# Performance work log

Measured on AMD Instinct MI355X. Metric: run time of the kernel, lower is better.

Reference implementation:

```python
import jax, jax.numpy as jnp
import numpy as np

C = 256
HEADS = 8
HEAD_DIM = C // HEADS
SCALE = HEAD_DIM ** -0.5
POOL = 2
LN_EPS = 1e-5


def setup_inputs() -> dict:
    key = jax.random.key(0)
    ks = jax.random.split(key, 10)
    B, H, W = 8, 64, 64
    std = 0.02
    return {
        "x": jax.random.normal(ks[0], (B, C, H, W), jnp.float32),
        "Wq": jax.random.normal(ks[1], (HEADS, C), jnp.float32) * std,
        "Wk": jax.random.normal(ks[2], (HEADS, C), jnp.float32) * std,
        "Wv": jax.random.normal(ks[3], (C, C), jnp.float32) * std,
        "Wsr": jax.random.normal(ks[4], (C, C), jnp.float32) * (2.0 / C) ** 0.5,
        "bsr": jnp.zeros((C,), jnp.float32),
        "gamma": jnp.ones((C,), jnp.float32),
        "beta": jnp.zeros((C,), jnp.float32),
        "Wp": jax.random.normal(ks[5], (C, C), jnp.float32) * std,
        "bp": jnp.zeros((C,), jnp.float32),
    }


def reference(x, Wq, Wk, Wv, Wsr, bsr, gamma, beta, Wp, bp):
    B, Cc, H, W = x.shape
    N = H * W
    # tokens [B, N, C]
    tok = x.reshape(B, Cc, N).transpose(0, 2, 1)
    # q: Linear(C -> heads), per-head scalar query  [B, heads, N]
    q = jnp.einsum("bnc,hc->bhn", tok, Wq)
    # spatial reduction: avgpool(pool_ratio) then 1x1 conv
    xp = x.reshape(B, Cc, H // POOL, POOL, W // POOL, POOL).mean(axis=(3, 5))
    xs = jnp.einsum("bchw,oc->bohw", xp, Wsr) + bsr[None, :, None, None]
    M = (H // POOL) * (W // POOL)
    x_ = xs.reshape(B, Cc, M).transpose(0, 2, 1)  # [B, M, C]
    # LayerNorm + GELU (exact erf, torch default)
    mu = x_.mean(-1, keepdims=True)
    var = ((x_ - mu) ** 2).mean(-1, keepdims=True)
    x_ = (x_ - mu) * jax.lax.rsqrt(var + LN_EPS) * gamma + beta
    x_ = jax.nn.gelu(x_, approximate=False)
    # k: per-head scalar key [B, heads, M]; v: [B, heads, M, head_dim]
    k = jnp.einsum("bmc,hc->bhm", x_, Wk)
    v = jnp.einsum("bmc,oc->bmo", x_, Wv).reshape(B, M, HEADS, HEAD_DIM).transpose(0, 2, 1, 3)
    # rank-1 attention scores [B, heads, N, M]
    attn = jax.nn.softmax(q[:, :, :, None] * k[:, :, None, :] * SCALE, axis=-1)
    out = jnp.einsum("bhnm,bhmd->bhnd", attn, v)  # [B, heads, N, head_dim]
    out = out.transpose(0, 2, 1, 3).reshape(B, N, Cc)
    out = out @ Wp.T + bp
    return out.transpose(0, 2, 1).reshape(B, Cc, H, W)
```

## Files before the change

### kernel.cpp

```cpp
#include <hip/hip_runtime.h>
#include <math.h>


#define NH 8
#define NJ 8
#define NT (NH * NJ)
#define SCALE 0.17677669529663687f

__device__ __constant__ float INVFACT[NJ] = {
    1.0f, 1.0f, 0.5f, 1.6666666666666666e-01f, 4.1666666666666664e-02f,
    8.3333333333333332e-03f, 1.3888888888888889e-03f, 1.9841269841269841e-04f};

__global__ void k0_q_prep(const float* __restrict__ x, const float* __restrict__ Wq,
                          const float* __restrict__ Wsr, const float* __restrict__ Wv,
                          float* __restrict__ q01, float* __restrict__ WsrT,
                          float* __restrict__ WvT) {
    __shared__ float wq[NH * 128];
    const int tid = threadIdx.x;
    const int blk = blockIdx.x;
    if (blk < 256) {
        const int b = blk >> 5, half = (blk >> 4) & 1, nt = blk & 15;
#pragma unroll
        for (int r = 0; r < 4; ++r) {
            int idx = r * 256 + tid;
            int h = idx >> 7, cc = idx & 127;
            wq[idx] = Wq[h * 256 + half * 128 + cc];
        }
        __syncthreads();
        const int n = nt * 256 + tid;
        const float* xb = x + (((size_t)b << 8) + half * 128) * 4096 + n;
        float acc[NH] = {};
#pragma unroll 8
        for (int c = 0; c < 128; ++c) {
            float xv = xb[(size_t)c << 12];
#pragma unroll
            for (int h = 0; h < NH; ++h) acc[h] += xv * wq[h * 128 + c];
        }
#pragma unroll
        for (int h = 0; h < NH; ++h)
            q01[((size_t)(half * 64 + b * 8 + h) << 12) + n] = acc[h];
    } else {
        const float* W = (blk < 288) ? Wsr : Wv;
        float* WT = (blk < 288) ? WsrT : WvT;
        const int c0 = (blk & 31) * 8;
#pragma unroll
        for (int r = 0; r < 2; ++r) {
            int fidx = r * 256 + tid;
            int c = c0 + (fidx >> 6), o4 = (fidx & 63) * 4;
            float4 t;
            t.x = W[(size_t)(o4 + 0) * 256 + c];
            t.y = W[(size_t)(o4 + 1) * 256 + c];
            t.z = W[(size_t)(o4 + 2) * 256 + c];
            t.w = W[(size_t)(o4 + 3) * 256 + c];
            *(float4*)&WT[(size_t)c * 256 + o4] = t;
        }
    }
}

__global__ __launch_bounds__(512, 1) void ka_mega(
        const float* __restrict__ x, const float* __restrict__ WsrT,
        const float* __restrict__ bsr, const float* __restrict__ WvT,
        const float* __restrict__ gamma, const float* __restrict__ beta,
        const float* __restrict__ Wk,
        float* __restrict__ Mpart, float* __restrict__ Spart) {
    __shared__ float smem[28800];
    float* a_pool = smem;
    float* wpan   = smem + 1152;
    float* g_lds  = smem + 9472;
    float* g_t    = smem + 17792;
    float4* wkv   = (float4*)(smem + 25984);
    float4* glv   = (float4*)(smem + 28032);
    float4* blv   = (float4*)(smem + 28288);
    float* klds   = smem + 28544;

    const int tid = threadIdx.x;
    const int blk = blockIdx.x;
    const int b = blk >> 5, mt = blk & 31;
    const int i2 = mt;

    const int ccs = tid >> 3, jg = tid & 7;
    const int mg = tid & 7, og = tid >> 3;

    wkv[tid] = ((const float4*)Wk)[tid];
    if (tid < 64) {
        glv[tid] = ((const float4*)gamma)[tid];
        blv[tid] = ((const float4*)beta)[tid];
    }

    float acc[4][4] = {};
    for (int c0 = 0; c0 < 256; c0 += 32) {
        __syncthreads();
        if (tid < 256) {
            const float* p = x + ((size_t)(b * 256 + c0 + ccs) << 12) +
                             i2 * 128 + jg * 8;
            float4 r00 = *(const float4*)p;
            float4 r01 = *(const float4*)(p + 4);
            float4 r10 = *(const float4*)(p + 64);
            float4 r11 = *(const float4*)(p + 68);
            float4 pv;
            pv.x = 0.25f * ((r00.x + r00.y) + (r10.x + r10.y));
            pv.y = 0.25f * ((r00.z + r00.w) + (r10.z + r10.w));
            pv.z = 0.25f * ((r01.x + r01.y) + (r11.x + r11.y));
            pv.w = 0.25f * ((r01.z + r01.w) + (r11.z + r11.w));
            *(float4*)&a_pool[ccs * 36 + jg * 4] = pv;
        }
#pragma unroll
        for (int r = 0; r < 4; ++r) {
            int fidx = r * 512 + tid;
            int cc = fidx >> 6, o4 = (fidx & 63) * 4;
            *(float4*)&wpan[cc * 260 + o4] =
                *(const float4*)&WsrT[(size_t)(c0 + cc) * 256 + o4];
        }
        __syncthreads();
#pragma unroll
        for (int cc = 0; cc < 32; ++cc) {
            float4 av = *(const float4*)&a_pool[cc * 36 + mg * 4];
            float4 bv = *(const float4*)&wpan[cc * 260 + og * 4];
            float am[4] = {av.x, av.y, av.z, av.w};
            float bo[4] = {bv.x, bv.y, bv.z, bv.w};
#pragma unroll
            for (int i = 0; i < 4; ++i)
#pragma unroll
                for (int j = 0; j < 4; ++j) acc[i][j] += am[i] * bo[j];
        }
    }
    {
        float4 bs = *(const float4*)&bsr[og * 4];
#pragma unroll
        for (int i = 0; i < 4; ++i) {
            float4 w0;
            w0.x = acc[i][0] + bs.x; w0.y = acc[i][1] + bs.y;
            w0.z = acc[i][2] + bs.z; w0.w = acc[i][3] + bs.w;
            *(float4*)&g_lds[(mg * 4 + i) * 260 + og * 4] = w0;
        }
    }
    __syncthreads();

    const int wave = tid >> 6, lane = tid & 63;
    {
        const float4 g4 = glv[lane], be4 = blv[lane];
        float4 wkreg[NH];
#pragma unroll
        for (int h = 0; h < NH; ++h) wkreg[h] = wkv[h * 64 + lane];
        const int w2 = wave >> 1, h2 = wave & 1;
        const int s = lane & 7;
        const int cb = ((w2 ^ (s >> 1)) << 3) | ((s & 1) << 2);
        const int cbh = cb ^ (h2 << 2);
        const int r0 = (lane * 4) << 5;
        float4 gg4[4];
#pragma unroll
        for (int ti = 0; ti < 4; ++ti) {
            const int mm = wave * 4 + ti;
            float4 vv = *(const float4*)&g_lds[mm * 260 + lane * 4];
            float ssum = (vv.x + vv.y) + (vv.z + vv.w);
            float s2 = (vv.x * vv.x + vv.y * vv.y) + (vv.z * vv.z + vv.w * vv.w);
#pragma unroll
            for (int off = 1; off < 64; off <<= 1) {
                ssum += __shfl_xor(ssum, off);
                s2 += __shfl_xor(s2, off);
            }
            const float mu = ssum * (1.f / 256.f);
            const float rstd = rsqrtf(s2 * (1.f / 256.f) - mu * mu + 1e-5f);
            float4 gg;
            {
                float xh;
                xh = (vv.x - mu) * rstd * g4.x + be4.x;
                gg.x = 0.5f * xh * (1.f + erff(xh * 0.70710678118654752f));
                xh = (vv.y - mu) * rstd * g4.y + be4.y;
                gg.y = 0.5f * xh * (1.f + erff(xh * 0.70710678118654752f));
                xh = (vv.z - mu) * rstd * g4.z + be4.z;
                gg.z = 0.5f * xh * (1.f + erff(xh * 0.70710678118654752f));
                xh = (vv.w - mu) * rstd * g4.w + be4.w;
                gg.w = 0.5f * xh * (1.f + erff(xh * 0.70710678118654752f));
            }
            gg4[ti] = gg;
            float acck[NH];
#pragma unroll
            for (int h = 0; h < NH; ++h) {
                float4 w = wkreg[h];
                acck[h] = (gg.x * w.x + gg.y * w.y) + (gg.z * w.z + gg.w * w.w);
            }
#pragma unroll
            for (int off = 1; off < 64; off <<= 1)
#pragma unroll
                for (int h = 0; h < NH; ++h) acck[h] += __shfl_xor(acck[h], off);
            if (lane == 0) {
#pragma unroll
                for (int h = 0; h < NH; ++h) klds[h * 32 + mm] = acck[h];
            }
        }
        float4 t;
#define GT_WRITE(K, COMP)                                                   \
        t.x = gg4[0].COMP; t.y = gg4[1].COMP;                               \
        t.z = gg4[2].COMP; t.w = gg4[3].COMP;                               \
        *(float4*)&g_t[r0 + ((K) << 5) + cbh] = t;
        GT_WRITE(0, x) GT_WRITE(1, y) GT_WRITE(2, z) GT_WRITE(3, w)
#undef GT_WRITE
    }

    float accv[4][4] = {};
    for (int c0 = 0; c0 < 256; c0 += 32) {
        __syncthreads();
#pragma unroll
        for (int r = 0; r < 4; ++r) {
            int fidx = r * 512 + tid;
            int cc = fidx >> 6, o4 = (fidx & 63) * 4;
            *(float4*)&wpan[cc * 260 + o4] =
                *(const float4*)&WvT[(size_t)(c0 + cc) * 256 + o4];
        }
        __syncthreads();
#pragma unroll
        for (int cc = 0; cc < 32; ++cc) {
            const int c = c0 + cc;
            const int swzc = ((c >> 2) & 7) << 2;
            float4 av = *(const float4*)&g_t[(c << 5) + ((mg << 2) ^ swzc)];
            float4 bv = *(const float4*)&wpan[cc * 260 + og * 4];
            float am[4] = {av.x, av.y, av.z, av.w};
            float bo[4] = {bv.x, bv.y, bv.z, bv.w};
#pragma unroll
            for (int i = 0; i < 4; ++i)
#pragma unroll
                for (int j = 0; j < 4; ++j) accv[i][j] += am[i] * bo[j];
        }
    }

    {
        const int h = og >> 3;
        float km[4], pw[4];
#pragma unroll
        for (int i = 0; i < 4; ++i) {
            km[i] = klds[h * 32 + mg * 4 + i];
            pw[i] = 1.f;
        }
        float sacc[NJ];
        float* Mrow = Mpart + ((size_t)blk << 11) + og * 4;
#pragma unroll
        for (int j = 0; j < NJ; ++j) {
            float mo[4];
#pragma unroll
            for (int o = 0; o < 4; ++o)
                mo[o] = (pw[0] * accv[0][o] + pw[1] * accv[1][o]) +
                        (pw[2] * accv[2][o] + pw[3] * accv[3][o]);
            float sj = (pw[0] + pw[1]) + (pw[2] + pw[3]);
#pragma unroll
            for (int i = 0; i < 4; ++i) pw[i] *= km[i];
#pragma unroll
            for (int off = 1; off < 8; off <<= 1) {
#pragma unroll
                for (int o = 0; o < 4; ++o) mo[o] += __shfl_xor(mo[o], off);
                sj += __shfl_xor(sj, off);
            }
            sacc[j] = sj;
            if (mg == 0) {
                float4 w0;
                w0.x = mo[0]; w0.y = mo[1]; w0.z = mo[2]; w0.w = mo[3];
                *(float4*)&Mrow[j * 256] = w0;
            }
        }
        if (mg == 0 && (og & 7) == 0) {
            float* Srow = Spart + ((size_t)blk << 6) + h * 8;
            float4 s0, s1;
            s0.x = sacc[0]; s0.y = sacc[1]; s0.z = sacc[2]; s0.w = sacc[3];
            s1.x = sacc[4]; s1.y = sacc[5]; s1.z = sacc[6]; s1.w = sacc[7];
            *(float4*)&Srow[0] = s0;
            *(float4*)&Srow[4] = s1;
        }
    }
}

__global__ void kc_fold(const float* __restrict__ Mpart,
                        const float* __restrict__ Spart,
                        const float* __restrict__ Wp,
                        float* __restrict__ P, float* __restrict__ S2) {
    const int bh = blockIdx.x;
    const int h = bh & 7, b = bh >> 3;
    const int tid = threadIdx.x;
    __shared__ float Ms[NJ][33];
    {
        const int j = tid >> 5, d = tid & 31;
        const float* src = Mpart + (((size_t)(b * 32) * 8 + j) << 8) + h * 32 + d;
        float s = 0.f;
#pragma unroll 8
        for (int mtn = 0; mtn < 32; ++mtn) s += src[(size_t)mtn << 11];
        Ms[j][d] = s * INVFACT[j];
    }
    if (tid < NJ) {
        const float* src = Spart + ((size_t)(b * 32) << 6) + h * 8 + tid;
        float ss = 0.f;
#pragma unroll 8
        for (int mtn = 0; mtn < 32; ++mtn) ss += src[mtn << 6];
        S2[bh * NJ + tid] = ss * INVFACT[tid];
    }
    __syncthreads();
    const int c = tid;
    float wp[32];
    const float* wrow = Wp + c * 256 + h * 32;
#pragma unroll
    for (int i = 0; i < 8; ++i) {
        float4 t = *(const float4*)(wrow + i * 4);
        wp[i * 4 + 0] = t.x; wp[i * 4 + 1] = t.y;
        wp[i * 4 + 2] = t.z; wp[i * 4 + 3] = t.w;
    }
#pragma unroll
    for (int j = 0; j < NJ; ++j) {
        float s = 0.f;
#pragma unroll
        for (int dd = 0; dd < 32; ++dd) s += wp[dd] * Ms[j][dd];
        P[((size_t)bh * NJ + j) * 256 + c] = s;
    }
}

__global__ void kd_out(const float* __restrict__ q01, const float* __restrict__ S2,
                       const float* __restrict__ P, const float* __restrict__ bp,
                       float* __restrict__ out) {
    __shared__ float p_lds[NT * 264];
    __shared__ float coef_lds[NT * 32];
    __shared__ float s2l[NT];
    const int tid = threadIdx.x;
    const int b = blockIdx.x >> 7, nt = blockIdx.x & 127;
    const int n0 = nt * 32;
    if (tid < NT) s2l[tid] = S2[b * NT + tid];
    const float* Pb = P + (size_t)b * (NT * 256);
#pragma unroll
    for (int r = 0; r < 16; ++r) {
        int fidx = r * 256 + tid;
        int t = fidx >> 6, c4 = (fidx & 63) * 4;
        *(float4*)&p_lds[t * 264 + c4] = *(const float4*)&Pb[t * 256 + c4];
    }
    __syncthreads();
    {
        const int n = tid & 31, h = tid >> 5;
        size_t qi = ((size_t)(b * NH + h) << 12) + n0 + n;
        float a = (q01[qi] + q01[qi + ((size_t)64 << 12)]) * SCALE;
        float den = s2l[h * NJ + NJ - 1];
#pragma unroll
        for (int j = NJ - 2; j >= 0; --j) den = den * a + s2l[h * NJ + j];
        float p = 1.0f / den;
#pragma unroll
        for (int j = 0; j < NJ; ++j) {
            coef_lds[(h * NJ + j) * 32 + n] = p;
            p *= a;
        }
    }
    __syncthreads();
    const int ng = tid & 7, og = tid >> 3;
    float acc[8][4] = {};
#pragma unroll 8
    for (int t = 0; t < NT; ++t) {
        float4 nv = *(const float4*)&coef_lds[t * 32 + ng * 4];
        float4 cv0 = *(const float4*)&p_lds[t * 264 + og * 8];
        float4 cv1 = *(const float4*)&p_lds[t * 264 + og * 8 + 4];
        float nm[4] = {nv.x, nv.y, nv.z, nv.w};
        float cm[8] = {cv0.x, cv0.y, cv0.z, cv0.w, cv1.x, cv1.y, cv1.z, cv1.w};
#pragma unroll
        for (int i = 0; i < 8; ++i)
#pragma unroll
            for (int j = 0; j < 4; ++j) acc[i][j] += cm[i] * nm[j];
    }
    float* ob = out + ((size_t)(b << 8) + og * 8) * 4096 + n0 + ng * 4;
#pragma unroll
    for (int i = 0; i < 8; ++i) {
        float bpc = bp[og * 8 + i];
        float4 r;
        r.x = acc[i][0] + bpc; r.y = acc[i][1] + bpc;
        r.z = acc[i][2] + bpc; r.w = acc[i][3] + bpc;
        *(float4*)(ob + (size_t)i * 4096) = r;
    }
}

extern "C" void kernel_launch(void* const* d_in, const int* in_sizes, int n_in,
                              void* d_out, int out_size, void* d_ws, size_t ws_size,
                              hipStream_t stream) {
    const float* x     = (const float*)d_in[0];
    const float* Wq    = (const float*)d_in[1];
    const float* Wk    = (const float*)d_in[2];
    const float* Wv    = (const float*)d_in[3];
    const float* Wsr   = (const float*)d_in[4];
    const float* bsr   = (const float*)d_in[5];
    const float* gamma = (const float*)d_in[6];
    const float* beta  = (const float*)d_in[7];
    const float* Wp    = (const float*)d_in[8];
    const float* bp    = (const float*)d_in[9];
    float* out = (float*)d_out;

    float* ws    = (float*)d_ws;
    float* Mpart = ws;
    float* Spart = Mpart + 524288;
    float* q01   = Spart + 16384;
    float* P     = q01 + 524288;
    float* S2    = P + 131072;
    float* WsrT  = S2 + 512;
    float* WvT   = WsrT + 65536;

    k0_q_prep<<<320, 256, 0, stream>>>(x, Wq, Wsr, Wv, q01, WsrT, WvT);
    ka_mega<<<256, 512, 0, stream>>>(x, WsrT, bsr, WvT, gamma, beta, Wk,
                                     Mpart, Spart);
    kc_fold<<<64, 256, 0, stream>>>(Mpart, Spart, Wp, P, S2);
    kd_out<<<1024, 256, 0, stream>>>(q01, S2, P, bp, out);
}
```

Measured before the change: 191.5 us.

## Split ka_mega into 512 half-tile blocks of 256 threads

```diff
diff --git a/kernel.cpp b/kernel.cpp
--- a/kernel.cpp
+++ b/kernel.cpp
@@ -57,56 +57,54 @@
     }
 }
 
-__global__ __launch_bounds__(512, 1) void ka_mega(
+__global__ __launch_bounds__(256, 2) void ka_mega(
         const float* __restrict__ x, const float* __restrict__ WsrT,
         const float* __restrict__ bsr, const float* __restrict__ WvT,
         const float* __restrict__ gamma, const float* __restrict__ beta,
         const float* __restrict__ Wk,
         float* __restrict__ Mpart, float* __restrict__ Spart) {
-    __shared__ float smem[28800];
-    float* a_pool = smem;
-    float* wpan   = smem + 1152;
-    float* g_lds  = smem + 9472;
-    float* g_t    = smem + 17792;
-    float4* wkv   = (float4*)(smem + 25984);
-    float4* glv   = (float4*)(smem + 28032);
-    float4* blv   = (float4*)(smem + 28288);
-    float* klds   = smem + 28544;
+    __shared__ float smem[19904];
+    float* wpan   = smem;
+    float* a_pool = smem + 8320;
+    float* g_lds  = smem + 8960;
+    float* g_t    = smem + 13120;
+    float4* wkv   = (float4*)(smem + 17216);
+    float4* glv   = (float4*)(smem + 19264);
+    float4* blv   = (float4*)(smem + 19520);
+    float* klds   = smem + 19776;
 
     const int tid = threadIdx.x;
     const int blk = blockIdx.x;
-    const int b = blk >> 5, mt = blk & 31;
-    const int i2 = mt;
+    const int b = blk >> 6, t16 = blk & 63;
+    const int pr = t16 >> 1, half = t16 & 1;
 
     const int ccs = tid >> 3, jg = tid & 7;
-    const int mg = tid & 7, og = tid >> 3;
+    const int mg = tid & 3, og = tid >> 2;
 
     wkv[tid] = ((const float4*)Wk)[tid];
+    wkv[256 + tid] = ((const float4*)Wk)[256 + tid];
     if (tid < 64) {
         glv[tid] = ((const float4*)gamma)[tid];
         blv[tid] = ((const float4*)beta)[tid];
     }
 
+    const size_t xoff = (size_t)pr * 128 + half * 32 + jg * 4;
+
     float acc[4][4] = {};
     for (int c0 = 0; c0 < 256; c0 += 32) {
         __syncthreads();
-        if (tid < 256) {
-            const float* p = x + ((size_t)(b * 256 + c0 + ccs) << 12) +
-                             i2 * 128 + jg * 8;
-            float4 r00 = *(const float4*)p;
-            float4 r01 = *(const float4*)(p + 4);
-            float4 r10 = *(const float4*)(p + 64);
-            float4 r11 = *(const float4*)(p + 68);
-            float4 pv;
-            pv.x = 0.25f * ((r00.x + r00.y) + (r10.x + r10.y));
-            pv.y = 0.25f * ((r00.z + r00.w) + (r10.z + r10.w));
-            pv.z = 0.25f * ((r01.x + r01.y) + (r11.x + r11.y));
-            pv.w = 0.25f * ((r01.z + r01.w) + (r11.z + r11.w));
-            *(float4*)&a_pool[ccs * 36 + jg * 4] = pv;
-        }
-#pragma unroll
-        for (int r = 0; r < 4; ++r) {
-            int fidx = r * 512 + tid;
+        {
+            const float* p = x + ((size_t)(b * 256 + c0 + ccs) << 12) + xoff;
+            float4 r0 = *(const float4*)p;
+            float4 r1 = *(const float4*)(p + 64);
+            float2 pv;
+            pv.x = 0.25f * ((r0.x + r0.y) + (r1.x + r1.y));
+            pv.y = 0.25f * ((r0.z + r0.w) + (r1.z + r1.w));
+            *(float2*)&a_pool[ccs * 20 + jg * 2] = pv;
+        }
+#pragma unroll
+        for (int r = 0; r < 8; ++r) {
+            int fidx = r * 256 + tid;
             int cc = fidx >> 6, o4 = (fidx & 63) * 4;
             *(float4*)&wpan[cc * 260 + o4] =
                 *(const float4*)&WsrT[(size_t)(c0 + cc) * 256 + o4];
@@ -114,7 +112,7 @@
         __syncthreads();
 #pragma unroll
         for (int cc = 0; cc < 32; ++cc) {
-            float4 av = *(const float4*)&a_pool[cc * 36 + mg * 4];
+            float4 av = *(const float4*)&a_pool[cc * 20 + mg * 4];
             float4 bv = *(const float4*)&wpan[cc * 260 + og * 4];
             float am[4] = {av.x, av.y, av.z, av.w};
             float bo[4] = {bv.x, bv.y, bv.z, bv.w};
@@ -142,11 +140,8 @@
         float4 wkreg[NH];
 #pragma unroll
         for (int h = 0; h < NH; ++h) wkreg[h] = wkv[h * 64 + lane];
-        const int w2 = wave >> 1, h2 = wave & 1;
-        const int s = lane & 7;
-        const int cb = ((w2 ^ (s >> 1)) << 3) | ((s & 1) << 2);
-        const int cbh = cb ^ (h2 << 2);
-        const int r0 = (lane * 4) << 5;
+        const int cbh = ((wave ^ (lane & 3)) << 2);
+        const int r0 = lane << 6;
         float4 gg4[4];
 #pragma unroll
         for (int ti = 0; ti < 4; ++ti) {
@@ -186,14 +181,14 @@
                 for (int h = 0; h < NH; ++h) acck[h] += __shfl_xor(acck[h], off);
             if (lane == 0) {
 #pragma unroll
-                for (int h = 0; h < NH; ++h) klds[h * 32 + mm] = acck[h];
+                for (int h = 0; h < NH; ++h) klds[h * 16 + mm] = acck[h];
             }
         }
         float4 t;
 #define GT_WRITE(K, COMP)                                                   \
         t.x = gg4[0].COMP; t.y = gg4[1].COMP;                               \
         t.z = gg4[2].COMP; t.w = gg4[3].COMP;                               \
-        *(float4*)&g_t[r0 + ((K) << 5) + cbh] = t;
+        *(float4*)&g_t[r0 + ((K) << 4) + cbh] = t;
         GT_WRITE(0, x) GT_WRITE(1, y) GT_WRITE(2, z) GT_WRITE(3, w)
 #undef GT_WRITE
     }
@@ -202,8 +197,8 @@
     for (int c0 = 0; c0 < 256; c0 += 32) {
         __syncthreads();
 #pragma unroll
-        for (int r = 0; r < 4; ++r) {
-            int fidx = r * 512 + tid;
+        for (int r = 0; r < 8; ++r) {
+            int fidx = r * 256 + tid;
             int cc = fidx >> 6, o4 = (fidx & 63) * 4;
             *(float4*)&wpan[cc * 260 + o4] =
                 *(const float4*)&WvT[(size_t)(c0 + cc) * 256 + o4];
@@ -212,8 +207,8 @@
 #pragma unroll
         for (int cc = 0; cc < 32; ++cc) {
             const int c = c0 + cc;
-            const int swzc = ((c >> 2) & 7) << 2;
-            float4 av = *(const float4*)&g_t[(c << 5) + ((mg << 2) ^ swzc)];
+            const int swzc = ((c >> 2) & 3) << 2;
+            float4 av = *(const float4*)&g_t[(c << 4) + ((mg << 2) ^ swzc)];
             float4 bv = *(const float4*)&wpan[cc * 260 + og * 4];
             float am[4] = {av.x, av.y, av.z, av.w};
             float bo[4] = {bv.x, bv.y, bv.z, bv.w};
@@ -229,7 +224,7 @@
         float km[4], pw[4];
 #pragma unroll
         for (int i = 0; i < 4; ++i) {
-            km[i] = klds[h * 32 + mg * 4 + i];
+            km[i] = klds[h * 16 + mg * 4 + i];
             pw[i] = 1.f;
         }
         float sacc[NJ];
@@ -245,7 +240,7 @@
 #pragma unroll
             for (int i = 0; i < 4; ++i) pw[i] *= km[i];
 #pragma unroll
-            for (int off = 1; off < 8; off <<= 1) {
+            for (int off = 1; off < 4; off <<= 1) {
 #pragma unroll
                 for (int o = 0; o < 4; ++o) mo[o] += __shfl_xor(mo[o], off);
                 sj += __shfl_xor(sj, off);
@@ -278,17 +273,17 @@
     __shared__ float Ms[NJ][33];
     {
         const int j = tid >> 5, d = tid & 31;
-        const float* src = Mpart + (((size_t)(b * 32) * 8 + j) << 8) + h * 32 + d;
+        const float* src = Mpart + (((size_t)(b * 64) * 8 + j) << 8) + h * 32 + d;
         float s = 0.f;
 #pragma unroll 8
-        for (int mtn = 0; mtn < 32; ++mtn) s += src[(size_t)mtn << 11];
+        for (int mtn = 0; mtn < 64; ++mtn) s += src[(size_t)mtn << 11];
         Ms[j][d] = s * INVFACT[j];
     }
     if (tid < NJ) {
-        const float* src = Spart + ((size_t)(b * 32) << 6) + h * 8 + tid;
+        const float* src = Spart + ((size_t)(b * 64) << 6) + h * 8 + tid;
         float ss = 0.f;
 #pragma unroll 8
-        for (int mtn = 0; mtn < 32; ++mtn) ss += src[mtn << 6];
+        for (int mtn = 0; mtn < 64; ++mtn) ss += src[mtn << 6];
         S2[bh * NJ + tid] = ss * INVFACT[tid];
     }
     __syncthreads();
@@ -385,15 +380,15 @@
 
     float* ws    = (float*)d_ws;
     float* Mpart = ws;
-    float* Spart = Mpart + 524288;
-    float* q01   = Spart + 16384;
+    float* Spart = Mpart + 1048576;
+    float* q01   = Spart + 32768;
     float* P     = q01 + 524288;
     float* S2    = P + 131072;
     float* WsrT  = S2 + 512;
     float* WvT   = WsrT + 65536;
 
     k0_q_prep<<<320, 256, 0, stream>>>(x, Wq, Wsr, Wv, q01, WsrT, WvT);
-    ka_mega<<<256, 512, 0, stream>>>(x, WsrT, bsr, WvT, gamma, beta, Wk,
+    ka_mega<<<512, 256, 0, stream>>>(x, WsrT, bsr, WvT, gamma, beta, Wk,
                                      Mpart, Spart);
     kc_fold<<<64, 256, 0, stream>>>(Mpart, Spart, Wp, P, S2);
     kd_out<<<1024, 256, 0, stream>>>(q01, S2, P, bp, out);
```

Result: no change. 190.6 us (-0.5%).
